# Kernel tuning notes

Hardware: AMD Instinct MI355X
Metric: run time of the kernel (lower is better)

Reference implementation:

```python
import jax, jax.numpy as jnp
import numpy as np

PLANE_DIMIDS = [(0, 1), (0, 2), (1, 2)]


def _grid_sample_bilinear(plane, gx, gy):
    """plane: (C,H,W); gx,gy: (B,) in [-1,1]; align_corners=True bilinear.
    gx indexes width (last axis), gy indexes height. Returns (C,B)."""
    C, H, W = plane.shape
    px = (gx + 1.0) * 0.5 * (W - 1)
    py = (gy + 1.0) * 0.5 * (H - 1)
    x0 = jnp.floor(px)
    y0 = jnp.floor(py)
    wx = px - x0  # frac weights
    wy = py - y0
    x0i = jnp.clip(x0.astype(jnp.int32), 0, W - 1)
    y0i = jnp.clip(y0.astype(jnp.int32), 0, H - 1)
    x1i = jnp.clip(x0i + 1, 0, W - 1)
    y1i = jnp.clip(y0i + 1, 0, H - 1)
    p00 = plane[:, y0i, x0i]  # (C,B)
    p01 = plane[:, y0i, x1i]
    p10 = plane[:, y1i, x0i]
    p11 = plane[:, y1i, x1i]
    return (p00 * (1 - wx) * (1 - wy) + p01 * wx * (1 - wy)
            + p10 * (1 - wx) * wy + p11 * wx * wy)


def setup_inputs() -> dict:
    key = jax.random.key(0)
    k0, k1, k2, k3 = jax.random.split(key, 4)
    B, C, R = 2_000_000, 16, 512
    init_bound = float(np.power(0.001, 1.0 / 3.0))
    x = jax.random.uniform(k0, (B, 3), dtype=jnp.float32, minval=-1.0, maxval=1.0)
    plane0 = jax.random.uniform(k1, (1, C, R, R), dtype=jnp.float32, minval=-init_bound, maxval=init_bound)
    plane1 = jax.random.uniform(k2, (1, C, R, R), dtype=jnp.float32, minval=-init_bound, maxval=init_bound)
    plane2 = jax.random.uniform(k3, (1, C, R, R), dtype=jnp.float32, minval=-init_bound, maxval=init_bound)
    return {"x": x, "plane0": plane0, "plane1": plane1, "plane2": plane2}


def reference(x, plane0, plane1, plane2):
    planes = [plane0[0], plane1[0], plane2[0]]  # drop leading batch dim -> (C,H,W)
    feats = None
    for (d0, d1), plane in zip(PLANE_DIMIDS, planes):
        # torch grid: grid[...,0]->width(x), grid[...,1]->height(y)
        f2d = _grid_sample_bilinear(plane, x[:, d0], x[:, d1])  # (C,B)
        feats = f2d if feats is None else feats * f2d
    return feats.T  # (B,C)
```

## Files before the change

kernel.cpp:

```cpp
#include <hip/hip_runtime.h>
#include <hip/hip_fp16.h>
#include <cstdint>
#include <cstddef>

constexpr int R  = 512;
constexpr int C  = 16;
constexpr int HW = R * R;

constexpr int NB9   = 512;
constexpr int NPART = 8;
constexpr int NCNT  = NB9 * NPART;
constexpr int CHUNK = 4096;
constexpr int KMAX  = 16;

typedef float v4f __attribute__((ext_vector_type(4)));
typedef int   v4i __attribute__((ext_vector_type(4)));

__device__ __forceinline__ float tcoord(float g) {
    return __fmul_rn(__fadd_rn(g, 1.0f), 255.5f);
}
__device__ __forceinline__ int cell512(float g) {
    const int i = (int)tcoord(g);
    return min(max(i, 0), R - 1);
}
__device__ __forceinline__ uint32_t mortonN(int a, int b, int c, int nb) {
    uint32_t k = 0;
#pragma unroll
    for (int i = 0; i < 5; ++i) {
        if (i < nb) {
            k |= ((uint32_t)((a >> i) & 1)) << (3 * i + 2);
            k |= ((uint32_t)((b >> i) & 1)) << (3 * i + 1);
            k |= ((uint32_t)((c >> i) & 1)) << (3 * i + 0);
        }
    }
    return k;
}
__device__ __forceinline__ uint32_t key9(float a, float b, float c) {
    return mortonN(cell512(a) >> 6, cell512(b) >> 6, cell512(c) >> 6, 3);
}

__device__ __forceinline__ v4i gload16(const void* base, uint32_t voff) {
    v4i r;
    asm volatile("global_load_dwordx4 %0, %1, %2"
                 : "=&v"(r) : "v"(voff), "s"(base));
    return r;
}
#define VMWAIT(N) do { \
    asm volatile("s_waitcnt vmcnt(" #N ")" ::: "memory"); \
    __builtin_amdgcn_sched_barrier(0); \
} while (0)

__global__ __launch_bounds__(256) void transpose_chw_hwc_h(
    const float* __restrict__ p0, const float* __restrict__ p1,
    const float* __restrict__ p2, __half* __restrict__ dst)
{
    __shared__ float lds[64 * 17];
    const int y  = blockIdx.x;
    const int x0 = blockIdx.y * 64;
    const int pl = blockIdx.z;
    const float* src = (pl == 0) ? p0 : ((pl == 1) ? p1 : p2);
    const int tid = threadIdx.x;
    const int xl  = tid & 63;
    const int c0  = tid >> 6;
#pragma unroll
    for (int i = 0; i < 4; ++i) {
        const int c = c0 * 4 + i;
        lds[xl * 17 + c] = src[c * HW + y * R + x0 + xl];
    }
    __syncthreads();
    __half2* dbase = (__half2*)(dst + ((size_t)pl * HW + (size_t)(y * R + x0)) * C);
#pragma unroll
    for (int i = 0; i < 2; ++i) {
        const int j  = tid + i * 256;
        const int e0 = 2 * j;
        const float a = lds[(e0 >> 4) * 17 + (e0 & 15)];
        const float b = lds[(e0 >> 4) * 17 + ((e0 & 15) + 1)];
        dbase[j] = __floats2half2_rn(a, b);
    }
}

__global__ __launch_bounds__(256) void hist_pts(
    const float* __restrict__ x, unsigned int* __restrict__ counts, int B)
{
    __shared__ unsigned int h[NB9];
    const int tid = threadIdx.x;
    for (int i = tid; i < NB9; i += 256) h[i] = 0;
    __syncthreads();
    const int start = blockIdx.x * CHUNK;
#pragma unroll
    for (int j = 0; j < CHUNK / 256; ++j) {
        const int i = start + j * 256 + tid;
        if (i < B) {
            const float a = x[(size_t)i * 3 + 0];
            const float b = x[(size_t)i * 3 + 1];
            const float c = x[(size_t)i * 3 + 2];
            atomicAdd(&h[key9(a, b, c)], 1u);
        }
    }
    __syncthreads();
    unsigned int* cb = counts + (blockIdx.x & (NPART - 1)) * NB9;
    for (int i = tid; i < NB9; i += 256) {
        const unsigned int c = h[i];
        if (c) atomicAdd(&cb[i], c);
    }
}

__global__ __launch_bounds__(1024) void scan_counts(
    const unsigned int* __restrict__ counts, unsigned int* __restrict__ cursor,
    unsigned int* __restrict__ binStart)
{
    __shared__ unsigned int s[1024];
    const int t = threadIdx.x;
    unsigned int v[4];
    unsigned int sum = 0;
#pragma unroll
    for (int i = 0; i < 4; ++i) {
        const int L = t * 4 + i;
        const int key = L >> 3, part = L & 7;
        v[i] = counts[part * NB9 + key];
        sum += v[i];
    }
    unsigned int run = 0;
#pragma unroll
    for (int i = 0; i < 4; ++i) { const unsigned int tmp = v[i]; v[i] = run; run += tmp; }
    s[t] = sum;
    __syncthreads();
    unsigned int incl = sum;
    for (int off = 1; off < 1024; off <<= 1) {
        const unsigned int u = (t >= off) ? s[t - off] : 0u;
        __syncthreads();
        incl += u;
        s[t] = incl;
        __syncthreads();
    }
    const unsigned int excl = incl - sum;
#pragma unroll
    for (int i = 0; i < 4; ++i) {
        const int L = t * 4 + i;
        const int key = L >> 3, part = L & 7;
        cursor[part * NB9 + key] = excl + v[i];
        if (part == 0) binStart[key] = excl + v[i];
    }
    if (t == 1023) binStart[NB9] = incl;
}

__global__ __launch_bounds__(256) void scatter_pts(
    const float* __restrict__ x, unsigned int* __restrict__ cursor,
    int4* __restrict__ recs, int B)
{
    __shared__ unsigned int h[NB9];
    __shared__ unsigned int gbase[NB9];
    __shared__ unsigned int lpre[NB9];
    __shared__ unsigned int lcur[NB9];
    __shared__ int4 buf[CHUNK];
    __shared__ unsigned short binOf[CHUNK];

    const int tid   = threadIdx.x;
    const int start = blockIdx.x * CHUNK;
    const int V     = min(CHUNK, B - start);

    for (int i = tid; i < NB9; i += 256) h[i] = 0;
    __syncthreads();

    float pa[CHUNK / 256], pb_[CHUNK / 256], pc[CHUNK / 256];
    unsigned int pk[CHUNK / 256];
#pragma unroll
    for (int j = 0; j < CHUNK / 256; ++j) {
        const int i = start + j * 256 + tid;
        pk[j] = 0xFFFFFFFFu;
        if (i < B) {
            pa[j] = x[(size_t)i * 3 + 0];
            pb_[j] = x[(size_t)i * 3 + 1];
            pc[j] = x[(size_t)i * 3 + 2];
            pk[j] = key9(pa[j], pb_[j], pc[j]);
            atomicAdd(&h[pk[j]], 1u);
        }
    }
    __syncthreads();

    unsigned int* cb = cursor + (blockIdx.x & (NPART - 1)) * NB9;
    for (int b = tid; b < NB9; b += 256) {
        const unsigned int c = h[b];
        gbase[b] = c ? atomicAdd(&cb[b], c) : 0u;
    }
    if (tid < 64) {
        unsigned int loc[8];
        unsigned int tot = 0;
#pragma unroll
        for (int j = 0; j < 8; ++j) { loc[j] = h[tid * 8 + j]; tot += loc[j]; }
        unsigned int run = tot;
#pragma unroll
        for (int d = 1; d < 64; d <<= 1) {
            const unsigned int u = __shfl_up(run, (unsigned)d, 64);
            if (tid >= d) run += u;
        }
        unsigned int excl = run - tot;
#pragma unroll
        for (int j = 0; j < 8; ++j) { lpre[tid * 8 + j] = excl; excl += loc[j]; }
    }
    __syncthreads();
    for (int b = tid; b < NB9; b += 256) lcur[b] = lpre[b];
    __syncthreads();

#pragma unroll
    for (int j = 0; j < CHUNK / 256; ++j) {
        if (pk[j] != 0xFFFFFFFFu) {
            const int i = start + j * 256 + tid;
            const unsigned int rk = atomicAdd(&lcur[pk[j]], 1u);
            buf[rk] = make_int4(__float_as_int(pa[j]), __float_as_int(pb_[j]),
                                __float_as_int(pc[j]), i);
            binOf[rk] = (unsigned short)pk[j];
        }
    }
    __syncthreads();

    for (int idx = tid; idx < V; idx += 256) {
        const int4 rc = buf[idx];
        const int  k  = binOf[idx];
        const unsigned int dest = gbase[k] + ((unsigned int)idx - lpre[k]);
        const v4i rv = { rc.x, rc.y, rc.z, rc.w };
        __builtin_nontemporal_store(rv, (v4i*)&recs[dest]);
    }
}

__global__ __launch_bounds__(512) void refine_pts(
    const unsigned int* __restrict__ binStart, int4* __restrict__ recs)
{
    __shared__ unsigned int h[64];
    __shared__ unsigned int pre[64];
    const int k = blockIdx.x;
    const unsigned int s0 = binStart[k];
    const unsigned int s1 = binStart[k + 1];
    const int tid = threadIdx.x;
    if (tid < 64) h[tid] = 0;
    __syncthreads();

    int4 rc[KMAX];
    unsigned int rs[KMAX];
#pragma unroll
    for (int j = 0; j < KMAX; ++j) {
        const unsigned int idx = s0 + (unsigned)tid + (unsigned)j * 512u;
        rs[j] = 0xFFFFFFFFu;
        if (idx < s1) {
            rc[j] = recs[idx];
            const int c0 = cell512(__int_as_float(rc[j].x)) >> 4;
            const int c1 = cell512(__int_as_float(rc[j].y)) >> 4;
            const int c2 = cell512(__int_as_float(rc[j].z)) >> 4;
            const unsigned int sub = mortonN(c0, c1, c2, 5) & 63u;
            const unsigned int rank = atomicAdd(&h[sub], 1u);
            rs[j] = (rank << 6) | sub;
        }
    }
    __syncthreads();

    if (tid < 64) {
        const unsigned int v = h[tid];
        unsigned int run = v;
#pragma unroll
        for (int d = 1; d < 64; d <<= 1) {
            const unsigned int u = __shfl_up(run, (unsigned)d, 64);
            if (tid >= d) run += u;
        }
        pre[tid] = run - v;
    }
    __syncthreads();

#pragma unroll
    for (int j = 0; j < KMAX; ++j) {
        if (rs[j] != 0xFFFFFFFFu) {
            const unsigned int sub  = rs[j] & 63u;
            const unsigned int rank = rs[j] >> 6;
            recs[s0 + pre[sub] + rank] = rc[j];
        }
    }
}

__global__ __launch_bounds__(256) void sample_sorted(
    const int4* __restrict__ recs, const __half* __restrict__ t,
    float* __restrict__ out, int B, int q, int r)
{
    const uint32_t bid  = blockIdx.x;
    const uint32_t xcd  = bid & 7u;
    const uint32_t slot = bid >> 3;
    const uint32_t base = (xcd < (uint32_t)r) ? xcd * (q + 1)
                                              : (uint32_t)r * (q + 1) + (xcd - r) * q;
    const uint32_t lb   = base + slot;

    const int tid = (int)(lb * 256u + threadIdx.x);
    const int p   = tid >> 1;
    const int h   = tid & 1;
    if (p >= B) return;

    const v4i rec = __builtin_nontemporal_load((const v4i*)&recs[p]);
    const float xv0 = __int_as_float(rec.x);
    const float xv1 = __int_as_float(rec.y);
    const float xv2 = __int_as_float(rec.z);

    float w[3][4];
    uint32_t off[3][4];
    const uint32_t hofs = (uint32_t)h * 16u;
#pragma unroll
    for (int pl = 0; pl < 3; ++pl) {
        const float gx = (pl == 2) ? xv1 : xv0;
        const float gy = (pl == 0) ? xv1 : xv2;
        const float px = (gx + 1.0f) * 0.5f * (float)(R - 1);
        const float py = (gy + 1.0f) * 0.5f * (float)(R - 1);
        const float x0f = floorf(px), y0f = floorf(py);
        const float wx = px - x0f,   wy = py - y0f;
        int x0 = (int)x0f; x0 = min(max(x0, 0), R - 1);
        int y0 = (int)y0f; y0 = min(max(y0, 0), R - 1);
        const int x1 = min(x0 + 1, R - 1);
        const int y1 = min(y0 + 1, R - 1);
        off[pl][0] = ((uint32_t)(y0 * R) + (uint32_t)x0) * 32u + hofs;
        off[pl][1] = ((uint32_t)(y0 * R) + (uint32_t)x1) * 32u + hofs;
        off[pl][2] = ((uint32_t)(y1 * R) + (uint32_t)x0) * 32u + hofs;
        off[pl][3] = ((uint32_t)(y1 * R) + (uint32_t)x1) * 32u + hofs;
        w[pl][0] = (1.f - wx) * (1.f - wy);
        w[pl][1] = wx * (1.f - wy);
        w[pl][2] = (1.f - wx) * wy;
        w[pl][3] = wx * wy;
    }

    v4i raw[3][4];
#pragma unroll
    for (int pl = 0; pl < 3; ++pl) {
        const void* pb = (const char*)t + (size_t)pl * ((size_t)HW * C * 2);
#pragma unroll
        for (int c2 = 0; c2 < 4; ++c2)
            raw[pl][c2] = gload16(pb, off[pl][c2]);
    }

    float acc[8] = {1.f, 1.f, 1.f, 1.f, 1.f, 1.f, 1.f, 1.f};

#pragma unroll
    for (int pl = 0; pl < 3; ++pl) {
        if (pl == 0) VMWAIT(8);
        else if (pl == 1) VMWAIT(4);
        else VMWAIT(0);
        const __half2* f0 = (const __half2*)&raw[pl][0];
        const __half2* f1 = (const __half2*)&raw[pl][1];
        const __half2* f2 = (const __half2*)&raw[pl][2];
        const __half2* f3 = (const __half2*)&raw[pl][3];
        const float w00 = w[pl][0], w01 = w[pl][1];
        const float w10 = w[pl][2], w11 = w[pl][3];
#pragma unroll
        for (int i2 = 0; i2 < 4; ++i2) {
            const float2 a0 = __half22float2(f0[i2]);
            const float2 a1 = __half22float2(f1[i2]);
            const float2 a2 = __half22float2(f2[i2]);
            const float2 a3 = __half22float2(f3[i2]);
            acc[2 * i2 + 0] *= a0.x * w00 + a1.x * w01 + a2.x * w10 + a3.x * w11;
            acc[2 * i2 + 1] *= a0.y * w00 + a1.y * w01 + a2.y * w10 + a3.y * w11;
        }
    }

    float* o = out + (size_t)rec.w * C + h * 8;
    const v4f o0 = { acc[0], acc[1], acc[2], acc[3] };
    const v4f o1 = { acc[4], acc[5], acc[6], acc[7] };
    __builtin_nontemporal_store(o0, (v4f*)(o + 0));
    __builtin_nontemporal_store(o1, (v4f*)(o + 4));
}

__global__ __launch_bounds__(256) void transpose_chw_hwc(
    const float* __restrict__ p0, const float* __restrict__ p1,
    const float* __restrict__ p2, float* __restrict__ dst)
{
    __shared__ float lds[64 * 17];
    const int y  = blockIdx.x;
    const int x0 = blockIdx.y * 64;
    const int pl = blockIdx.z;
    const float* src = (pl == 0) ? p0 : ((pl == 1) ? p1 : p2);
    const int tid = threadIdx.x;
    const int xl  = tid & 63;
    const int c0  = tid >> 6;
#pragma unroll
    for (int i = 0; i < 4; ++i) {
        const int c = c0 * 4 + i;
        lds[xl * 17 + c] = src[c * HW + y * R + x0 + xl];
    }
    __syncthreads();
    float* dbase = dst + ((size_t)pl * HW + (size_t)(y * R + x0)) * C;
#pragma unroll
    for (int i = 0; i < 4; ++i) {
        const int j = tid + i * 256;
        dbase[j] = lds[(j >> 4) * 17 + (j & 15)];
    }
}

__global__ __launch_bounds__(256) void sample_hwc(
    const float* __restrict__ x, const float* __restrict__ t,
    float* __restrict__ out, int B)
{
    const int tid = blockIdx.x * 256 + threadIdx.x;
    const int p   = tid >> 2;
    const int cg  = tid & 3;
    if (p >= B) return;

    const float xv0 = x[(size_t)p * 3 + 0];
    const float xv1 = x[(size_t)p * 3 + 1];
    const float xv2 = x[(size_t)p * 3 + 2];
    const float gxs[3] = { xv0, xv0, xv1 };
    const float gys[3] = { xv1, xv2, xv2 };
    float4 acc = make_float4(1.f, 1.f, 1.f, 1.f);

#pragma unroll
    for (int pl = 0; pl < 3; ++pl) {
        const float gx = gxs[pl], gy = gys[pl];
        const float px = (gx + 1.0f) * 0.5f * (float)(R - 1);
        const float py = (gy + 1.0f) * 0.5f * (float)(R - 1);
        const float x0f = floorf(px), y0f = floorf(py);
        const float wx = px - x0f,   wy = py - y0f;
        int x0 = (int)x0f; x0 = min(max(x0, 0), R - 1);
        int y0 = (int)y0f; y0 = min(max(y0, 0), R - 1);
        const int x1 = min(x0 + 1, R - 1);
        const int y1 = min(y0 + 1, R - 1);

        const float* pb = t + (size_t)pl * (size_t)(HW * C) + cg * 4;
        const float4 p00 = *(const float4*)(pb + (size_t)(y0 * R + x0) * C);
        const float4 p01 = *(const float4*)(pb + (size_t)(y0 * R + x1) * C);
        const float4 p10 = *(const float4*)(pb + (size_t)(y1 * R + x0) * C);
        const float4 p11 = *(const float4*)(pb + (size_t)(y1 * R + x1) * C);

        const float w00 = (1.f - wx) * (1.f - wy);
        const float w01 = wx * (1.f - wy);
        const float w10 = (1.f - wx) * wy;
        const float w11 = wx * wy;

        float4 fv;
        fv.x = p00.x * w00 + p01.x * w01 + p10.x * w10 + p11.x * w11;
        fv.y = p00.y * w00 + p01.y * w01 + p10.y * w10 + p11.y * w11;
        fv.z = p00.z * w00 + p01.z * w01 + p10.z * w10 + p11.z * w11;
        fv.w = p00.w * w00 + p01.w * w01 + p10.w * w10 + p11.w * w11;

        acc.x *= fv.x; acc.y *= fv.y; acc.z *= fv.z; acc.w *= fv.w;
    }

    *(float4*)(out + (size_t)p * C + cg * 4) = acc;
}

__global__ __launch_bounds__(256) void sample_chw(
    const float* __restrict__ x,
    const float* __restrict__ p0, const float* __restrict__ p1,
    const float* __restrict__ p2, float* __restrict__ out, int B)
{
    const int tid = blockIdx.x * 256 + threadIdx.x;
    const int p   = tid >> 2;
    const int cg  = tid & 3;
    if (p >= B) return;
    const float xv0 = x[(size_t)p * 3 + 0];
    const float xv1 = x[(size_t)p * 3 + 1];
    const float xv2 = x[(size_t)p * 3 + 2];
    const float gxs[3] = { xv0, xv0, xv1 };
    const float gys[3] = { xv1, xv2, xv2 };
    const float* planes[3] = { p0, p1, p2 };
    float acc[4] = {1.f, 1.f, 1.f, 1.f};
#pragma unroll
    for (int pl = 0; pl < 3; ++pl) {
        const float gx = gxs[pl], gy = gys[pl];
        const float px = (gx + 1.0f) * 0.5f * (float)(R - 1);
        const float py = (gy + 1.0f) * 0.5f * (float)(R - 1);
        const float x0f = floorf(px), y0f = floorf(py);
        const float wx = px - x0f,   wy = py - y0f;
        int x0 = (int)x0f; x0 = min(max(x0, 0), R - 1);
        int y0 = (int)y0f; y0 = min(max(y0, 0), R - 1);
        const int x1 = min(x0 + 1, R - 1);
        const int y1 = min(y0 + 1, R - 1);
        const float w00 = (1.f - wx) * (1.f - wy);
        const float w01 = wx * (1.f - wy);
        const float w10 = (1.f - wx) * wy;
        const float w11 = wx * wy;
        const float* pb = planes[pl];
#pragma unroll
        for (int k = 0; k < 4; ++k) {
            const int c = cg * 4 + k;
            const float* b2 = pb + (size_t)c * HW;
            const float v00 = b2[y0 * R + x0];
            const float v01 = b2[y0 * R + x1];
            const float v10 = b2[y1 * R + x0];
            const float v11 = b2[y1 * R + x1];
            acc[k] *= v00 * w00 + v01 * w01 + v10 * w10 + v11 * w11;
        }
    }
    float* o = out + (size_t)p * C + cg * 4;
    o[0] = acc[0]; o[1] = acc[1]; o[2] = acc[2]; o[3] = acc[3];
}

extern "C" void kernel_launch(void* const* d_in, const int* in_sizes, int n_in,
                              void* d_out, int out_size, void* d_ws, size_t ws_size,
                              hipStream_t stream) {
    const float* x  = (const float*)d_in[0];
    const float* p0 = (const float*)d_in[1];
    const float* p1 = (const float*)d_in[2];
    const float* p2 = (const float*)d_in[3];
    float* out = (float*)d_out;
    const int B = in_sizes[0] / 3;

    const size_t t_bytes    = (size_t)3 * HW * C * sizeof(__half);
    const size_t recs_bytes = (size_t)B * 16;
    const size_t cnt_bytes  = (size_t)NCNT * 4;
    const size_t bs_bytes   = (size_t)(NB9 + 1) * 4;

    const size_t off_t      = 0;
    const size_t off_recs   = (t_bytes + 255) & ~(size_t)255;
    const size_t off_counts = (off_recs + recs_bytes + 255) & ~(size_t)255;
    const size_t off_cursor = (off_counts + cnt_bytes + 255) & ~(size_t)255;
    const size_t off_bs     = (off_cursor + cnt_bytes + 255) & ~(size_t)255;
    const size_t need_full  = off_bs + bs_bytes;

    const size_t need_fp32  = (size_t)3 * HW * C * sizeof(float);

    if (d_ws != nullptr && ws_size >= need_full) {
        __half*       t      = (__half*)((char*)d_ws + off_t);
        int4*         recs   = (int4*)((char*)d_ws + off_recs);
        unsigned int* counts = (unsigned int*)((char*)d_ws + off_counts);
        unsigned int* cursor = (unsigned int*)((char*)d_ws + off_cursor);
        unsigned int* bstart = (unsigned int*)((char*)d_ws + off_bs);

        dim3 tg(R, R / 64, 3);
        transpose_chw_hwc_h<<<tg, 256, 0, stream>>>(p0, p1, p2, t);

        hipMemsetAsync(counts, 0, cnt_bytes, stream);
        const int nblkP = (B + CHUNK - 1) / CHUNK;
        hist_pts<<<nblkP, 256, 0, stream>>>(x, counts, B);
        scan_counts<<<1, 1024, 0, stream>>>(counts, cursor, bstart);
        scatter_pts<<<nblkP, 256, 0, stream>>>(x, cursor, recs, B);
        refine_pts<<<NB9, 512, 0, stream>>>(bstart, recs);

        const int nthr2 = 2 * B;
        const int nblk2 = (nthr2 + 255) / 256;
        const int q = nblk2 / 8, r = nblk2 % 8;
        sample_sorted<<<nblk2, 256, 0, stream>>>(recs, t, out, B, q, r);
    } else if (d_ws != nullptr && ws_size >= need_fp32) {
        float* tf = (float*)d_ws;
        dim3 tg(R, R / 64, 3);
        transpose_chw_hwc<<<tg, 256, 0, stream>>>(p0, p1, p2, tf);
        const int nthr = B * 4;
        const int nblk = (nthr + 255) / 256;
        sample_hwc<<<nblk, 256, 0, stream>>>(x, tf, out, B);
    } else {
        const int nthr = B * 4;
        const int nblk = (nthr + 255) / 256;
        sample_chw<<<nblk, 256, 0, stream>>>(x, p0, p1, p2, out, B);
    }
}
```

Baseline: 133.8 us.

## Fuse per-bin refine sort into the sampling kernel using an LDS order list

The separate refine_pts and sample_sorted kernels are merged into one sample_bin kernel, launched with one 512-thread block per coarse bin. Each block computes a 64-way Morton sub-bin ordering of its points into a shared-memory index list. It then loops over those points in that order to do the trilinear-plane gathers and write outputs. This removes the refine pass's global read and write of the record array and one launch. In exchange, only 512 persistent-style blocks do all sampling, which lowers the number of waves available to hide gather latency. Bins larger than the shared-memory capacity fall back to unsorted order for the overflow points.

```diff
diff --git a/kernel.cpp b/kernel.cpp
--- a/kernel.cpp
+++ b/kernel.cpp
@@ -11,7 +11,8 @@
 constexpr int NPART = 8;
 constexpr int NCNT  = NB9 * NPART;
 constexpr int CHUNK = 4096;
-constexpr int KMAX  = 16;
+constexpr int KMX   = 9;
+constexpr int KCAP  = KMX * 512;
 
 typedef float v4f __attribute__((ext_vector_type(4)));
 typedef int   v4i __attribute__((ext_vector_type(4)));
@@ -223,38 +224,46 @@
     }
 }
 
-__global__ __launch_bounds__(512) void refine_pts(
-    const unsigned int* __restrict__ binStart, int4* __restrict__ recs)
-{
-    __shared__ unsigned int h[64];
+__global__ __launch_bounds__(512) void sample_bin(
+    const int4* __restrict__ recs, const __half* __restrict__ t,
+    const unsigned int* __restrict__ binStart,
+    float* __restrict__ out, int B)
+{
+    __shared__ unsigned int hh[64];
     __shared__ unsigned int pre[64];
-    const int k = blockIdx.x;
+    __shared__ unsigned short order[KCAP];
+
+    const unsigned int bid = blockIdx.x;
+    const int k = (int)((bid & 7u) * (NB9 / 8u) + (bid >> 3));
     const unsigned int s0 = binStart[k];
     const unsigned int s1 = binStart[k + 1];
+    const int n = (int)(s1 - s0);
+    if (n <= 0) return;
+    const int ns = min(n, KCAP);
     const int tid = threadIdx.x;
-    if (tid < 64) h[tid] = 0;
-    __syncthreads();
-
-    int4 rc[KMAX];
-    unsigned int rs[KMAX];
-#pragma unroll
-    for (int j = 0; j < KMAX; ++j) {
-        const unsigned int idx = s0 + (unsigned)tid + (unsigned)j * 512u;
+
+    if (tid < 64) hh[tid] = 0;
+    __syncthreads();
+
+    unsigned int rs[KMX];
+#pragma unroll
+    for (int j = 0; j < KMX; ++j) {
+        const int idx = tid + j * 512;
         rs[j] = 0xFFFFFFFFu;
-        if (idx < s1) {
-            rc[j] = recs[idx];
-            const int c0 = cell512(__int_as_float(rc[j].x)) >> 4;
-            const int c1 = cell512(__int_as_float(rc[j].y)) >> 4;
-            const int c2 = cell512(__int_as_float(rc[j].z)) >> 4;
+        if (idx < ns) {
+            const v4i rc = *(const v4i*)&recs[s0 + idx];
+            const int c0 = cell512(__int_as_float(rc.x)) >> 4;
+            const int c1 = cell512(__int_as_float(rc.y)) >> 4;
+            const int c2 = cell512(__int_as_float(rc.z)) >> 4;
             const unsigned int sub = mortonN(c0, c1, c2, 5) & 63u;
-            const unsigned int rank = atomicAdd(&h[sub], 1u);
+            const unsigned int rank = atomicAdd(&hh[sub], 1u);
             rs[j] = (rank << 6) | sub;
         }
     }
     __syncthreads();
 
     if (tid < 64) {
-        const unsigned int v = h[tid];
+        const unsigned int v = hh[tid];
         unsigned int run = v;
 #pragma unroll
         for (int d = 1; d < 64; d <<= 1) {
@@ -266,99 +275,87 @@
     __syncthreads();
 
 #pragma unroll
-    for (int j = 0; j < KMAX; ++j) {
+    for (int j = 0; j < KMX; ++j) {
         if (rs[j] != 0xFFFFFFFFu) {
             const unsigned int sub  = rs[j] & 63u;
             const unsigned int rank = rs[j] >> 6;
-            recs[s0 + pre[sub] + rank] = rc[j];
-        }
-    }
-}
-
-__global__ __launch_bounds__(256) void sample_sorted(
-    const int4* __restrict__ recs, const __half* __restrict__ t,
-    float* __restrict__ out, int B, int q, int r)
-{
-    const uint32_t bid  = blockIdx.x;
-    const uint32_t xcd  = bid & 7u;
-    const uint32_t slot = bid >> 3;
-    const uint32_t base = (xcd < (uint32_t)r) ? xcd * (q + 1)
-                                              : (uint32_t)r * (q + 1) + (xcd - r) * q;
-    const uint32_t lb   = base + slot;
-
-    const int tid = (int)(lb * 256u + threadIdx.x);
-    const int p   = tid >> 1;
-    const int h   = tid & 1;
-    if (p >= B) return;
-
-    const v4i rec = __builtin_nontemporal_load((const v4i*)&recs[p]);
-    const float xv0 = __int_as_float(rec.x);
-    const float xv1 = __int_as_float(rec.y);
-    const float xv2 = __int_as_float(rec.z);
-
-    float w[3][4];
-    uint32_t off[3][4];
-    const uint32_t hofs = (uint32_t)h * 16u;
-#pragma unroll
-    for (int pl = 0; pl < 3; ++pl) {
-        const float gx = (pl == 2) ? xv1 : xv0;
-        const float gy = (pl == 0) ? xv1 : xv2;
-        const float px = (gx + 1.0f) * 0.5f * (float)(R - 1);
-        const float py = (gy + 1.0f) * 0.5f * (float)(R - 1);
-        const float x0f = floorf(px), y0f = floorf(py);
-        const float wx = px - x0f,   wy = py - y0f;
-        int x0 = (int)x0f; x0 = min(max(x0, 0), R - 1);
-        int y0 = (int)y0f; y0 = min(max(y0, 0), R - 1);
-        const int x1 = min(x0 + 1, R - 1);
-        const int y1 = min(y0 + 1, R - 1);
-        off[pl][0] = ((uint32_t)(y0 * R) + (uint32_t)x0) * 32u + hofs;
-        off[pl][1] = ((uint32_t)(y0 * R) + (uint32_t)x1) * 32u + hofs;
-        off[pl][2] = ((uint32_t)(y1 * R) + (uint32_t)x0) * 32u + hofs;
-        off[pl][3] = ((uint32_t)(y1 * R) + (uint32_t)x1) * 32u + hofs;
-        w[pl][0] = (1.f - wx) * (1.f - wy);
-        w[pl][1] = wx * (1.f - wy);
-        w[pl][2] = (1.f - wx) * wy;
-        w[pl][3] = wx * wy;
-    }
-
-    v4i raw[3][4];
-#pragma unroll
-    for (int pl = 0; pl < 3; ++pl) {
-        const void* pb = (const char*)t + (size_t)pl * ((size_t)HW * C * 2);
-#pragma unroll
-        for (int c2 = 0; c2 < 4; ++c2)
-            raw[pl][c2] = gload16(pb, off[pl][c2]);
-    }
-
-    float acc[8] = {1.f, 1.f, 1.f, 1.f, 1.f, 1.f, 1.f, 1.f};
-
-#pragma unroll
-    for (int pl = 0; pl < 3; ++pl) {
-        if (pl == 0) VMWAIT(8);
-        else if (pl == 1) VMWAIT(4);
-        else VMWAIT(0);
-        const __half2* f0 = (const __half2*)&raw[pl][0];
-        const __half2* f1 = (const __half2*)&raw[pl][1];
-        const __half2* f2 = (const __half2*)&raw[pl][2];
-        const __half2* f3 = (const __half2*)&raw[pl][3];
-        const float w00 = w[pl][0], w01 = w[pl][1];
-        const float w10 = w[pl][2], w11 = w[pl][3];
-#pragma unroll
-        for (int i2 = 0; i2 < 4; ++i2) {
-            const float2 a0 = __half22float2(f0[i2]);
-            const float2 a1 = __half22float2(f1[i2]);
-            const float2 a2 = __half22float2(f2[i2]);
-            const float2 a3 = __half22float2(f3[i2]);
-            acc[2 * i2 + 0] *= a0.x * w00 + a1.x * w01 + a2.x * w10 + a3.x * w11;
-            acc[2 * i2 + 1] *= a0.y * w00 + a1.y * w01 + a2.y * w10 + a3.y * w11;
-        }
-    }
-
-    float* o = out + (size_t)rec.w * C + h * 8;
-    const v4f o0 = { acc[0], acc[1], acc[2], acc[3] };
-    const v4f o1 = { acc[4], acc[5], acc[6], acc[7] };
-    __builtin_nontemporal_store(o0, (v4f*)(o + 0));
-    __builtin_nontemporal_store(o1, (v4f*)(o + 4));
+            order[pre[sub] + rank] = (unsigned short)(tid + j * 512);
+        }
+    }
+    __syncthreads();
+
+    for (int s2 = tid; s2 < 2 * n; s2 += 512) {
+        const int sp = s2 >> 1;
+        const int h  = s2 & 1;
+        const int ri = (sp < ns) ? (int)order[sp] : sp;
+        const v4i rec = *(const v4i*)&recs[s0 + ri];
+        const float xv0 = __int_as_float(rec.x);
+        const float xv1 = __int_as_float(rec.y);
+        const float xv2 = __int_as_float(rec.z);
+
+        float w[3][4];
+        uint32_t off[3][4];
+        const uint32_t hofs = (uint32_t)h * 16u;
+#pragma unroll
+        for (int pl = 0; pl < 3; ++pl) {
+            const float gx = (pl == 2) ? xv1 : xv0;
+            const float gy = (pl == 0) ? xv1 : xv2;
+            const float px = (gx + 1.0f) * 0.5f * (float)(R - 1);
+            const float py = (gy + 1.0f) * 0.5f * (float)(R - 1);
+            const float x0f = floorf(px), y0f = floorf(py);
+            const float wx = px - x0f,   wy = py - y0f;
+            int x0 = (int)x0f; x0 = min(max(x0, 0), R - 1);
+            int y0 = (int)y0f; y0 = min(max(y0, 0), R - 1);
+            const int x1 = min(x0 + 1, R - 1);
+            const int y1 = min(y0 + 1, R - 1);
+            off[pl][0] = ((uint32_t)(y0 * R) + (uint32_t)x0) * 32u + hofs;
+            off[pl][1] = ((uint32_t)(y0 * R) + (uint32_t)x1) * 32u + hofs;
+            off[pl][2] = ((uint32_t)(y1 * R) + (uint32_t)x0) * 32u + hofs;
+            off[pl][3] = ((uint32_t)(y1 * R) + (uint32_t)x1) * 32u + hofs;
+            w[pl][0] = (1.f - wx) * (1.f - wy);
+            w[pl][1] = wx * (1.f - wy);
+            w[pl][2] = (1.f - wx) * wy;
+            w[pl][3] = wx * wy;
+        }
+
+        v4i raw[3][4];
+#pragma unroll
+        for (int pl = 0; pl < 3; ++pl) {
+            const void* pb = (const char*)t + (size_t)pl * ((size_t)HW * C * 2);
+#pragma unroll
+            for (int c2 = 0; c2 < 4; ++c2)
+                raw[pl][c2] = gload16(pb, off[pl][c2]);
+        }
+
+        float acc[8] = {1.f, 1.f, 1.f, 1.f, 1.f, 1.f, 1.f, 1.f};
+#pragma unroll
+        for (int pl = 0; pl < 3; ++pl) {
+            if (pl == 0) VMWAIT(8);
+            else if (pl == 1) VMWAIT(4);
+            else VMWAIT(0);
+            const __half2* f0 = (const __half2*)&raw[pl][0];
+            const __half2* f1 = (const __half2*)&raw[pl][1];
+            const __half2* f2 = (const __half2*)&raw[pl][2];
+            const __half2* f3 = (const __half2*)&raw[pl][3];
+            const float w00 = w[pl][0], w01 = w[pl][1];
+            const float w10 = w[pl][2], w11 = w[pl][3];
+#pragma unroll
+            for (int i2 = 0; i2 < 4; ++i2) {
+                const float2 a0 = __half22float2(f0[i2]);
+                const float2 a1 = __half22float2(f1[i2]);
+                const float2 a2 = __half22float2(f2[i2]);
+                const float2 a3 = __half22float2(f3[i2]);
+                acc[2 * i2 + 0] *= a0.x * w00 + a1.x * w01 + a2.x * w10 + a3.x * w11;
+                acc[2 * i2 + 1] *= a0.y * w00 + a1.y * w01 + a2.y * w10 + a3.y * w11;
+            }
+        }
+
+        float* o = out + (size_t)rec.w * C + h * 8;
+        const v4f o0 = { acc[0], acc[1], acc[2], acc[3] };
+        const v4f o1 = { acc[4], acc[5], acc[6], acc[7] };
+        __builtin_nontemporal_store(o0, (v4f*)(o + 0));
+        __builtin_nontemporal_store(o1, (v4f*)(o + 4));
+    }
 }
 
 __global__ __launch_bounds__(256) void transpose_chw_hwc(
@@ -524,12 +521,8 @@
         hist_pts<<<nblkP, 256, 0, stream>>>(x, counts, B);
         scan_counts<<<1, 1024, 0, stream>>>(counts, cursor, bstart);
         scatter_pts<<<nblkP, 256, 0, stream>>>(x, cursor, recs, B);
-        refine_pts<<<NB9, 512, 0, stream>>>(bstart, recs);
-
-        const int nthr2 = 2 * B;
-        const int nblk2 = (nthr2 + 255) / 256;
-        const int q = nblk2 / 8, r = nblk2 % 8;
-        sample_sorted<<<nblk2, 256, 0, stream>>>(recs, t, out, B, q, r);
+
+        sample_bin<<<NB9, 512, 0, stream>>>(recs, t, bstart, out, B);
     } else if (d_ws != nullptr && ws_size >= need_fp32) {
         float* tf = (float*)d_ws;
         dim3 tg(R, R / 64, 3);
```

Measured after the change: 146.4 us. +9.4%, slower.
